# Kernel tuning notes

Measured on AMD Instinct MI355X. Metric: run time of the kernel, lower is better.

## Reference

```python
import jax, jax.numpy as jnp
import numpy as np

NEG_INF = -1e30
EPS = 1e-7  # keras.backend.epsilon()


def _ctc_loss(y_true, y_pred):
    """Faithful CTC loss matching keras ctc_batch_cost + tf v1 ctc_loss.

    y_true: [B, L] int labels (no blanks), all rows full length L.
    y_pred: [B, T, C] probabilities; tf ctc_loss re-softmaxes log(p+eps).
    Blank index = C - 1. Returns loss [B, 1].
    """
    B, T, C = y_pred.shape
    L = y_true.shape[1]
    S = 2 * L + 1
    blank = C - 1

    # keras passes log(y_pred+eps) as logits; tf ctc_loss applies softmax
    lp = jax.nn.log_softmax(jnp.log(y_pred + EPS), axis=-1)  # [B,T,C]

    # extended label sequence: blank, l0, blank, l1, ..., blank  [B,S]
    ext = jnp.full((B, S), blank, dtype=y_true.dtype)
    ext = ext.at[:, 1::2].set(y_true)

    # skip transition (s-2 -> s) allowed iff ext[s] != blank and ext[s] != ext[s-2]
    same_as_2back = jnp.concatenate(
        [jnp.ones((B, 2), bool), ext[:, 2:] == ext[:, :-2]], axis=1)
    can_skip = (ext != blank) & (~same_as_2back)  # [B,S]

    # emission log-prob of each lattice state at each time: [B,T,S]
    lp_ext = jnp.take_along_axis(lp, ext[:, None, :], axis=2)

    # alpha init at t=0: only states 0 (blank) and 1 (first label) reachable
    alpha0 = jnp.full((B, S), NEG_INF, dtype=lp.dtype)
    alpha0 = alpha0.at[:, 0].set(lp_ext[:, 0, 0])
    alpha0 = alpha0.at[:, 1].set(lp_ext[:, 0, 1])

    pad1 = jnp.full((B, 1), NEG_INF, dtype=lp.dtype)
    pad2 = jnp.full((B, 2), NEG_INF, dtype=lp.dtype)

    def step(alpha, lp_t):
        a_stay = alpha
        a_prev = jnp.concatenate([pad1, alpha[:, :-1]], axis=1)
        a_skip = jnp.where(can_skip,
                           jnp.concatenate([pad2, alpha[:, :-2]], axis=1),
                           NEG_INF)
        m = jnp.maximum(a_stay, jnp.maximum(a_prev, a_skip))
        lse = m + jnp.log(jnp.exp(a_stay - m) + jnp.exp(a_prev - m)
                          + jnp.exp(a_skip - m))
        return lse + lp_t, None

    # scan over remaining T-1 time steps
    alphaT, _ = jax.lax.scan(step, alpha0, jnp.swapaxes(lp_ext, 0, 1)[1:])

    # total log-likelihood: end at last blank or last label
    loglik = jnp.logaddexp(alphaT[:, S - 1], alphaT[:, S - 2])
    return -loglik[:, None]  # [B,1], matches expand_dims(..., 1)


def setup_inputs() -> dict:
    key = jax.random.key(0)
    k1, k2 = jax.random.split(key)
    B, T, C, L = 128, 1024, 128, 128
    y_true = jax.random.randint(k1, (B, L), 0, C - 1, dtype=jnp.int32)
    y_pred = jax.random.uniform(k2, (B, T, C), dtype=jnp.float32)
    return {"y_true": y_true, "y_pred": y_pred}


def reference(y_true, y_pred):
    return _ctc_loss(y_true, y_pred)
```

## Files before the change

### kernel.cpp

```cpp
#include <hip/hip_runtime.h>

#define TT 1024
#define CC 128
#define LL 128
#define EPSF 1e-7f
#define LN2F 0.69314718055994531f

#define LOG2F(x) __builtin_amdgcn_logf(x)

typedef unsigned int uint;

template <int CTRL>
__device__ __forceinline__ int dpp_i(int old_, int x) {
  return __builtin_amdgcn_update_dpp(old_, x, CTRL, 0xf, 0xf, false);
}
template <int CTRL>
__device__ __forceinline__ float dpp0f(float x) {
  return __uint_as_float((uint)__builtin_amdgcn_update_dpp(
      0, (int)__float_as_uint(x), CTRL, 0xf, 0xf, true));
}
__device__ __forceinline__ float dpp_shr1_f32(float x) {
  return __uint_as_float((uint)__builtin_amdgcn_update_dpp(
      0, (int)__float_as_uint(x), 0x138, 0xf, 0xf, true));
}
__device__ __forceinline__ float readlane63_f(float v) {
  return __uint_as_float(
      (uint)__builtin_amdgcn_readlane((int)__float_as_uint(v), 63));
}

__device__ __forceinline__ uint bf16bits(float x) {
  uint u = __float_as_uint(x);
  return (u + 0x7fffu + ((u >> 16) & 1u)) >> 16;
}


#define CTC_STEP(wv, pbf)                                   \
  do {                                                      \
    const float p1 = __uint_as_float((wv) << 16);           \
    const float p2 = __uint_as_float((wv) & 0xffff0000u);   \
    const float pb = (pbf);                                 \
    const float p3 = dpp_shr1_f32(a3);                      \
    const float n0 = (a0 + p3) * pb;                        \
    const float n1 = __builtin_fmaf(s1f, p3, a0 + a1) * p1; \
    const float n2 = (a2 + a1) * pb;                        \
    const float n3 = __builtin_fmaf(s3f, a1, a3 + a2) * p2; \
    const float n4 = (a4 + a3) * pb;                        \
    a0 = n0; a1 = n1; a2 = n2; a3 = n3; a4 = n4;            \
  } while (0)

#define CTC_QUAD(et, eb)      \
  do {                        \
    CTC_STEP((et).x, (eb).x); \
    CTC_STEP((et).y, (eb).y); \
    CTC_STEP((et).z, (eb).z); \
    CTC_STEP((et).w, (eb).w); \
  } while (0)

#define CTC_RESCALE()                                                \
  do {                                                               \
    const float m = fmaxf(fmaxf(fmaxf(a0, a1), fmaxf(a2, a3)), a4);  \
    int ke = (int)(__float_as_uint(m) >> 23);                        \
    ke = max(ke, dpp_i<0x111>(ke, ke));                              \
    ke = max(ke, dpp_i<0x112>(ke, ke));                              \
    ke = max(ke, dpp_i<0x114>(ke, ke));                              \
    ke = max(ke, dpp_i<0x118>(ke, ke));                              \
    ke = max(ke, dpp_i<0x142>(ke, ke));                              \
    ke = max(ke, dpp_i<0x143>(ke, ke));                              \
    ke = __builtin_amdgcn_readlane(ke, 63);                          \
    int e = ke - 227;             \
    e = e < -127 ? -127 : e;                                         \
    const float sc = __uint_as_float((uint)(127 - e) << 23);         \
    a0 *= sc; a1 *= sc; a2 *= sc; a3 *= sc; a4 *= sc;                \
    ell += e;                                                        \
  } while (0)

#define ST_LOAD(S, qg)                                          \
  do {                                                          \
    const float* Pq = Pb + (size_t)(qg) * 4 * CC + 2 * L;       \
    vv##S##0 = *(const float2*)(Pq + 0 * CC);                   \
    vv##S##1 = *(const float2*)(Pq + 1 * CC);                   \
    vv##S##2 = *(const float2*)(Pq + 2 * CC);                   \
    vv##S##3 = *(const float2*)(Pq + 3 * CC);                   \
  } while (0)

#define ST_COMP(S, qg)                                                      \
  do {                                                                      \
    const float2 vr0 = vv##S##0, vr1 = vv##S##1;                            \
    const float2 vr2 = vv##S##2, vr3 = vv##S##3;                            \
    const float2 vr[4] = {vr0, vr1, vr2, vr3};                              \
    float ss[4];                                                            \
    ss[0] = (vr0.x + vr0.y) + (2.0f * EPSF);                                \
    ss[1] = (vr1.x + vr1.y) + (2.0f * EPSF);                                \
    ss[2] = (vr2.x + vr2.y) + (2.0f * EPSF);                                \
    ss[3] = (vr3.x + vr3.y) + (2.0f * EPSF);                                \
    _Pragma("unroll") for (int j = 0; j < 4; ++j)                           \
        ss[j] += dpp0f<0x111>(ss[j]);                        \
    _Pragma("unroll") for (int j = 0; j < 4; ++j)                           \
        ss[j] += dpp0f<0x112>(ss[j]);                        \
    _Pragma("unroll") for (int j = 0; j < 4; ++j)                           \
        ss[j] += dpp0f<0x114>(ss[j]);                        \
    _Pragma("unroll") for (int j = 0; j < 4; ++j)                           \
        ss[j] += dpp0f<0x118>(ss[j]);                        \
    _Pragma("unroll") for (int j = 0; j < 4; ++j)                           \
        ss[j] += dpp0f<0x142>(ss[j]);                      \
    _Pragma("unroll") for (int j = 0; j < 4; ++j)                           \
        ss[j] += dpp0f<0x143>(ss[j]);    \
    uint wds[4];                                                            \
    float nys[4];                                                           \
    _Pragma("unroll") for (int j = 0; j < 4; ++j) {                         \
      const float r = 1.0f / readlane63_f(ss[j]);                           \
      const float er = EPSF * r;                                            \
      const float nx = __builtin_fmaf(vr[j].x, r, er);                      \
      const float ny = __builtin_fmaf(vr[j].y, r, er);                      \
      const uint pk = (bf16bits(ny) << 16) | bf16bits(nx);                  \
      const uint wx = (uint)__builtin_amdgcn_ds_bpermute(gxb, (int)pk);     \
      const uint wy = (uint)__builtin_amdgcn_ds_bpermute(gyb, (int)pk);     \
      const uint bx = sx ? (wx >> 16) : (wx & 0xffffu);                     \
      const uint by = sy ? (wy >> 16) : (wy & 0xffffu);                     \
      wds[j] = (by << 16) | bx;                                             \
      nys[j] = ny;                                                          \
    }                                                                       \
    uint4 val;                                                              \
    val.x = wds[0]; val.y = wds[1]; val.z = wds[2]; val.w = wds[3];         \
    *(uint4*)((char*)ETl + (((qg) >> 3) & 3) * 8192 +                       \
              ((qg) & 7) * 1024 + L * 16) = val;                            \
    if (L == 63) {                                                          \
      float4 e4;                                                            \
      e4.x = nys[0]; e4.y = nys[1]; e4.z = nys[2]; e4.w = nys[3];           \
      *(float4*)&EBl[(qg) * 4] = e4;                                        \
    }                                                                       \
  } while (0)

#define LOADBUF(bb)                   \
  do {                                \
    const int qb = (bb) * 8 + w - 1;  \
    ST_LOAD(A, qb);                   \
    ST_LOAD(B, qb + 3);               \
    if (w < 3) ST_LOAD(C, qb + 6);    \
  } while (0)
#define COMPBUF(bb)                   \
  do {                                \
    const int qb = (bb) * 8 + w - 1;  \
    ST_COMP(A, qb);                   \
    ST_COMP(B, qb + 3);               \
    if (w < 3) ST_COMP(C, qb + 6);    \
  } while (0)

__global__ __launch_bounds__(256) void ctc_fused(const int* __restrict__ yt,
                                                 const float* __restrict__ yp,
                                                 float* __restrict__ out) {
  const int b = blockIdx.x;
  const int tid = threadIdx.x;
  const int L = tid & 63;
  const int w = tid >> 6;

  __shared__ uint4 ETl[4][8][64];
  __shared__ __align__(16) float EBl[TT];

  const int2 lab = *(const int2*)(yt + b * LL + 2 * L);

  const int labm1 = __shfl_up(lab.y, 1);
  const float s1f = ((L > 0) && (lab.x != labm1)) ? 1.0f : 0.0f;
  const float s3f = (lab.y != lab.x) ? 1.0f : 0.0f;

  const float* Pb = yp + (size_t)b * TT * CC;
  const int gxb = (lab.x >> 1) << 2, gyb = (lab.y >> 1) << 2;
  const int sx = lab.x & 1, sy = lab.y & 1;

  float2 vvA0, vvA1, vvA2, vvA3;
  float2 vvB0, vvB1, vvB2, vvB3;
  float2 vvC0, vvC1, vvC2, vvC3;

  if (w != 0) {
    LOADBUF(0);
    COMPBUF(0);
    LOADBUF(1);
    COMPBUF(1);
    LOADBUF(2);
  }
  __syncthreads();

  uint4 etA = {0, 0, 0, 0}, etB = {0, 0, 0, 0};
  float4 ebA = {0, 0, 0, 0}, ebB = {0, 0, 0, 0};
  if (w == 0) {
    etA = ((const uint4*)ETl)[L];
    ebA = *(const float4*)&EBl[0];
  }

  float a0 = (w == 0 && L == 0) ? 0x1.0p100f : 0.0f;
  float a1 = 0.0f, a2 = 0.0f, a3 = 0.0f, a4 = 0.0f;
  int ell = -100;

#pragma unroll 1
  for (int kk = 0; kk < 32; ++kk) {
    if (w == 0) {
      const uint4* cur = (const uint4*)ETl + (size_t)(kk & 3) * 512;
      const float4* ebp = (const float4*)&EBl[kk * 32];
      etB = cur[1 * 64 + L]; ebB = ebp[1];
      CTC_QUAD(etA, ebA);
      etA = cur[2 * 64 + L]; ebA = ebp[2];
      CTC_QUAD(etB, ebB);
      etB = cur[3 * 64 + L]; ebB = ebp[3];
      CTC_QUAD(etA, ebA);
      etA = cur[4 * 64 + L]; ebA = ebp[4];
      CTC_QUAD(etB, ebB);
      CTC_RESCALE();
      etB = cur[5 * 64 + L]; ebB = ebp[5];
      CTC_QUAD(etA, ebA);
      etA = cur[6 * 64 + L]; ebA = ebp[6];
      CTC_QUAD(etB, ebB);
      etB = cur[7 * 64 + L]; ebB = ebp[7];
      CTC_QUAD(etA, ebA);
      etA = ((const uint4*)ETl)[(size_t)((kk + 1) & 3) * 512 + L];
      ebA = *(const float4*)&EBl[(kk < 31) ? (kk + 1) * 32 : 1020];
      CTC_QUAD(etB, ebB);
      CTC_RESCALE();
    } else {
      if (kk < 30) COMPBUF(kk + 2);
      if (kk < 29) LOADBUF(kk + 3);
    }
    __syncthreads();
  }

  if (tid == 63) {
    float s = a3 + a4;
    if (s < 1e-37f) s = 1e-37f;
    out[b] = -LN2F * ((float)ell + LOG2F(s));
  }
}

extern "C" void kernel_launch(void* const* d_in, const int* in_sizes, int n_in,
                              void* d_out, int out_size, void* d_ws,
                              size_t ws_size, hipStream_t stream) {
  (void)d_ws; (void)ws_size; (void)n_in; (void)out_size;
  const int* yt = (const int*)d_in[0];
  const float* yp = (const float*)d_in[1];
  float* out = (float*)d_out;
  const int B = in_sizes[0] / LL;
  hipLaunchKernelGGL(ctc_fused, dim3(B), dim3(256), 0, stream, yt, yp, out);
}
```

Baseline: 131.4 us.

## Double-buffer producer register staging so global loads issue before compute

Producer waves now hold two sets of register staging buffers and alternate between them. The loop is unrolled by two so that each iteration issues the global loads for block kk+3 before computing and storing block kk+2 from the other buffer set. This gives the loads a full iteration of latency to hide behind, where before they had to complete in time for the next iteration's compute. The cost is higher register pressure in the producer waves, which may spill or lower occupancy.

```diff
diff --git a/kernel.cpp b/kernel.cpp
--- a/kernel.cpp
+++ b/kernel.cpp
@@ -131,19 +131,44 @@
     }                                                                       \
   } while (0)
 
-#define LOADBUF(bb)                   \
+#define LOADBUF3(X, Y, Z, bb)         \
   do {                                \
     const int qb = (bb) * 8 + w - 1;  \
-    ST_LOAD(A, qb);                   \
-    ST_LOAD(B, qb + 3);               \
-    if (w < 3) ST_LOAD(C, qb + 6);    \
-  } while (0)
-#define COMPBUF(bb)                   \
+    ST_LOAD(X, qb);                   \
+    ST_LOAD(Y, qb + 3);               \
+    if (w < 3) ST_LOAD(Z, qb + 6);    \
+  } while (0)
+#define COMPBUF3(X, Y, Z, bb)         \
   do {                                \
     const int qb = (bb) * 8 + w - 1;  \
-    ST_COMP(A, qb);                   \
-    ST_COMP(B, qb + 3);               \
-    if (w < 3) ST_COMP(C, qb + 6);    \
+    ST_COMP(X, qb);                   \
+    ST_COMP(Y, qb + 3);               \
+    if (w < 3) ST_COMP(Z, qb + 6);    \
+  } while (0)
+
+#define CONSUME(kk_)                                                     \
+  do {                                                                   \
+    const uint4* cur = (const uint4*)ETl + (size_t)((kk_) & 3) * 512;    \
+    const float4* ebp = (const float4*)&EBl[(kk_) * 32];                 \
+    etB = cur[1 * 64 + L]; ebB = ebp[1];                                 \
+    CTC_QUAD(etA, ebA);                                          \
+    etA = cur[2 * 64 + L]; ebA = ebp[2];                                 \
+    CTC_QUAD(etB, ebB);                                          \
+    etB = cur[3 * 64 + L]; ebB = ebp[3];                                 \
+    CTC_QUAD(etA, ebA);                                          \
+    etA = cur[4 * 64 + L]; ebA = ebp[4];                                 \
+    CTC_QUAD(etB, ebB);                                          \
+    CTC_RESCALE();                                                       \
+    etB = cur[5 * 64 + L]; ebB = ebp[5];                                 \
+    CTC_QUAD(etA, ebA);                                          \
+    etA = cur[6 * 64 + L]; ebA = ebp[6];                                 \
+    CTC_QUAD(etB, ebB);                                          \
+    etB = cur[7 * 64 + L]; ebB = ebp[7];                                 \
+    CTC_QUAD(etA, ebA);                                          \
+    etA = ((const uint4*)ETl)[(size_t)(((kk_) + 1) & 3) * 512 + L];      \
+    ebA = *(const float4*)&EBl[((kk_) < 31) ? ((kk_) + 1) * 32 : 1020];  \
+    CTC_QUAD(etB, ebB);                                          \
+    CTC_RESCALE();                                                       \
   } while (0)
 
 __global__ __launch_bounds__(256) void ctc_fused(const int* __restrict__ yt,
@@ -170,13 +195,16 @@
   float2 vvA0, vvA1, vvA2, vvA3;
   float2 vvB0, vvB1, vvB2, vvB3;
   float2 vvC0, vvC1, vvC2, vvC3;
+  float2 vvD0, vvD1, vvD2, vvD3;
+  float2 vvE0, vvE1, vvE2, vvE3;
+  float2 vvF0, vvF1, vvF2, vvF3;
 
   if (w != 0) {
-    LOADBUF(0);
-    COMPBUF(0);
-    LOADBUF(1);
-    COMPBUF(1);
-    LOADBUF(2);
+    LOADBUF3(A, B, C, 0);
+    COMPBUF3(A, B, C, 0);
+    LOADBUF3(A, B, C, 1);
+    COMPBUF3(A, B, C, 1);
+    LOADBUF3(A, B, C, 2);
   }
   __syncthreads();
 
@@ -192,32 +220,19 @@
   int ell = -100;
 
 #pragma unroll 1
-  for (int kk = 0; kk < 32; ++kk) {
+  for (int kk = 0; kk < 32; kk += 2) {
     if (w == 0) {
-      const uint4* cur = (const uint4*)ETl + (size_t)(kk & 3) * 512;
-      const float4* ebp = (const float4*)&EBl[kk * 32];
-      etB = cur[1 * 64 + L]; ebB = ebp[1];
-      CTC_QUAD(etA, ebA);
-      etA = cur[2 * 64 + L]; ebA = ebp[2];
-      CTC_QUAD(etB, ebB);
-      etB = cur[3 * 64 + L]; ebB = ebp[3];
-      CTC_QUAD(etA, ebA);
-      etA = cur[4 * 64 + L]; ebA = ebp[4];
-      CTC_QUAD(etB, ebB);
-      CTC_RESCALE();
-      etB = cur[5 * 64 + L]; ebB = ebp[5];
-      CTC_QUAD(etA, ebA);
-      etA = cur[6 * 64 + L]; ebA = ebp[6];
-      CTC_QUAD(etB, ebB);
-      etB = cur[7 * 64 + L]; ebB = ebp[7];
-      CTC_QUAD(etA, ebA);
-      etA = ((const uint4*)ETl)[(size_t)((kk + 1) & 3) * 512 + L];
-      ebA = *(const float4*)&EBl[(kk < 31) ? (kk + 1) * 32 : 1020];
-      CTC_QUAD(etB, ebB);
-      CTC_RESCALE();
+      CONSUME(kk);
     } else {
-      if (kk < 30) COMPBUF(kk + 2);
-      if (kk < 29) LOADBUF(kk + 3);
+      if (kk < 29) LOADBUF3(D, E, F, kk + 3);
+      if (kk < 30) COMPBUF3(A, B, C, kk + 2);
+    }
+    __syncthreads();
+    if (w == 0) {
+      CONSUME(kk + 1);
+    } else {
+      if (kk + 1 < 29) LOADBUF3(A, B, C, kk + 4);
+      if (kk + 1 < 30) COMPBUF3(D, E, F, kk + 3);
     }
     __syncthreads();
   }
```

New measurement: 132.2 us. About the same (+0.6%).
